# Optimization experiments

Hardware: AMD Instinct MI355X
Metric: run time of the kernel (lower is better)

## Reference

```python
import jax, jax.numpy as jnp
import numpy as np

N_NODES = 100000
N_EDGES = 600000
D_IN = 128
D_OUT = 512  # hidden_size * gates_num = 128 * 4


def setup_inputs() -> dict:
    key = jax.random.key(0)
    k1, k2, k3, k4 = jax.random.split(key, 4)
    x = jax.random.normal(k1, (N_NODES, D_IN), dtype=jnp.float32)
    edge_index = jax.random.randint(k2, (2, N_EDGES), 0, N_NODES, dtype=jnp.int64)
    W = jax.random.normal(k3, (D_OUT, D_IN), dtype=jnp.float32) * (1.0 / np.sqrt(D_IN))
    b = jax.random.normal(k4, (D_OUT,), dtype=jnp.float32) * 0.01
    return {"x": x, "edge_index": edge_index, "W": W, "b": b}


def reference(x, edge_index, W, b):
    row, col = edge_index[0], edge_index[1]
    # gather neighbor features and scatter-add into destination nodes
    agg = jax.ops.segment_sum(x[col], row, num_segments=x.shape[0])  # [N, D_IN]
    out = x + agg  # residual
    return out @ W.T + b  # [N, D_OUT]
```

## Files before the change

kernel.cpp:

```cpp
#include <hip/hip_runtime.h>
#include <hip/hip_bf16.h>

#define N_NODES 100000
#define N_EDGES 600000
#define D_IN 128
#define D_OUT 512
#define CAP 40
#define OVF_CAP 1024

typedef __bf16 bf16x8 __attribute__((ext_vector_type(8)));
typedef __bf16 bf16x2 __attribute__((ext_vector_type(2)));
typedef float f32x4 __attribute__((ext_vector_type(4)));

#define OFF_CNT   25600000
#define OFF_OVFC  26000000
#define OFF_OVF   26000016
#define OFF_BUCK  26008208

__global__ void k_bucket(const int* __restrict__ ei, int* __restrict__ cnt,
                         int* __restrict__ bucket, int* __restrict__ ovf_cnt,
                         int2* __restrict__ ovf) {
    int e = blockIdx.x * blockDim.x + threadIdx.x;
    if (e >= N_EDGES) return;
    int r = ei[e];
    int c = ei[N_EDGES + e];
    int slot = atomicAdd(&cnt[r], 1);
    if (slot < CAP) {
        bucket[(size_t)r * CAP + slot] = c;
    } else {
        int oi = atomicAdd(ovf_cnt, 1);
        if (oi < OVF_CAP) ovf[oi] = make_int2(r, c);
    }
}

__global__ void k_agg(const float* __restrict__ x, const int* __restrict__ cnt,
                      const int* __restrict__ bucket, const int* __restrict__ ovf_cnt,
                      const int2* __restrict__ ovf, __bf16* __restrict__ h) {
    int gw = (blockIdx.x * blockDim.x + threadIdx.x) >> 6;
    if (gw >= N_NODES) return;
    int lane = threadIdx.x & 63;
    const float2* xr = (const float2*)x;

    float2 a0 = xr[(size_t)gw * 64 + lane];
    float ax1 = 0.f, ay1 = 0.f, ax2 = 0.f, ay2 = 0.f, ax3 = 0.f, ay3 = 0.f;

    int deg = __builtin_amdgcn_readfirstlane(cnt[gw]);
    int dmin = deg < CAP ? deg : CAP;
    const int* bk = bucket + (size_t)gw * CAP;

    int myc = (lane < dmin) ? bk[lane] : 0;

    int d = 0;
    for (; d + 3 < dmin; d += 4) {
        int c0 = __builtin_amdgcn_readlane(myc, d);
        int c1 = __builtin_amdgcn_readlane(myc, d + 1);
        int c2 = __builtin_amdgcn_readlane(myc, d + 2);
        int c3 = __builtin_amdgcn_readlane(myc, d + 3);
        float2 v0 = xr[(size_t)c0 * 64 + lane];
        float2 v1 = xr[(size_t)c1 * 64 + lane];
        float2 v2 = xr[(size_t)c2 * 64 + lane];
        float2 v3 = xr[(size_t)c3 * 64 + lane];
        a0.x += v0.x; a0.y += v0.y;
        ax1 += v1.x;  ay1 += v1.y;
        ax2 += v2.x;  ay2 += v2.y;
        ax3 += v3.x;  ay3 += v3.y;
    }
    for (; d < dmin; ++d) {
        int c0 = __builtin_amdgcn_readlane(myc, d);
        float2 v0 = xr[(size_t)c0 * 64 + lane];
        a0.x += v0.x; a0.y += v0.y;
    }
    a0.x += ax1 + ax2 + ax3;
    a0.y += ay1 + ay2 + ay3;

    if (deg > CAP) {
        int n = *ovf_cnt;
        if (n > OVF_CAP) n = OVF_CAP;
        for (int i = 0; i < n; ++i) {
            int2 e = ovf[i];
            if (e.x == gw) {
                float2 v = xr[(size_t)e.y * 64 + lane];
                a0.x += v.x; a0.y += v.y;
            }
        }
    }

    bf16x2 o = { (__bf16)a0.x, (__bf16)a0.y };
    ((bf16x2*)h)[(size_t)gw * 64 + lane] = o;
}

#define BM 128
#define BN 128
#define LDA 136
#define LDB 136
#define NWG 3128

__device__ inline bf16x8 cvt8(float4 v0, float4 v1) {
    bf16x8 u = { (__bf16)v0.x, (__bf16)v0.y, (__bf16)v0.z, (__bf16)v0.w,
                 (__bf16)v1.x, (__bf16)v1.y, (__bf16)v1.z, (__bf16)v1.w };
    return u;
}

__launch_bounds__(512, 4)
__global__ void k_gemm(const __bf16* __restrict__ h, const float* __restrict__ W,
                       const float* __restrict__ bias, float* __restrict__ out) {
    __shared__ __bf16 As[BM * LDA];
    __shared__ __bf16 Bs[BN * LDB];

    int tid = threadIdx.x;

    int bid = blockIdx.x;
    int wg = (bid & 7) * (NWG / 8) + (bid >> 3);
    int m0 = (wg >> 2) * BM;
    int n0 = (wg & 3) * BN;

    #pragma unroll
    for (int it = 0; it < 4; ++it) {
        int i = tid + it * 512;
        int r = i >> 4;
        int c = (i & 15) << 3;
        int gr = m0 + r;
        if (gr > N_NODES - 1) gr = N_NODES - 1;
        *(bf16x8*)&As[r * LDA + c] = *(const bf16x8*)(h + (size_t)gr * D_IN + c);
    }
    #pragma unroll
    for (int it = 0; it < 4; ++it) {
        int i = tid + it * 512;
        int r = i >> 4;
        int c = (i & 15) << 3;
        const float* src = W + (size_t)(n0 + r) * D_IN + c;
        float4 v0 = *(const float4*)(src);
        float4 v1 = *(const float4*)(src + 4);
        *(bf16x8*)&Bs[r * LDB + c] = cvt8(v0, v1);
    }
    __syncthreads();

    int lane = tid & 63;
    int wave = tid >> 6;
    int wm = wave & 1;
    int wn = wave >> 1;
    int quad = lane >> 4;
    int l16 = lane & 15;

    f32x4 acc[4][2] = {};

    const __bf16* Abase = &As[(wm * 64 + l16) * LDA + quad * 8];
    const __bf16* Bbase = &Bs[(wn * 32 + l16) * LDB + quad * 8];

    #pragma unroll
    for (int ks = 0; ks < 4; ++ks) {
        bf16x8 a0 = *(const bf16x8*)(Abase + ks * 32);
        bf16x8 a1 = *(const bf16x8*)(Abase + 16 * LDA + ks * 32);
        bf16x8 a2 = *(const bf16x8*)(Abase + 32 * LDA + ks * 32);
        bf16x8 a3 = *(const bf16x8*)(Abase + 48 * LDA + ks * 32);
        bf16x8 b0 = *(const bf16x8*)(Bbase + ks * 32);
        bf16x8 b1 = *(const bf16x8*)(Bbase + 16 * LDB + ks * 32);
        acc[0][0] = __builtin_amdgcn_mfma_f32_16x16x32_bf16(a0, b0, acc[0][0], 0, 0, 0);
        acc[0][1] = __builtin_amdgcn_mfma_f32_16x16x32_bf16(a0, b1, acc[0][1], 0, 0, 0);
        acc[1][0] = __builtin_amdgcn_mfma_f32_16x16x32_bf16(a1, b0, acc[1][0], 0, 0, 0);
        acc[1][1] = __builtin_amdgcn_mfma_f32_16x16x32_bf16(a1, b1, acc[1][1], 0, 0, 0);
        acc[2][0] = __builtin_amdgcn_mfma_f32_16x16x32_bf16(a2, b0, acc[2][0], 0, 0, 0);
        acc[2][1] = __builtin_amdgcn_mfma_f32_16x16x32_bf16(a2, b1, acc[2][1], 0, 0, 0);
        acc[3][0] = __builtin_amdgcn_mfma_f32_16x16x32_bf16(a3, b0, acc[3][0], 0, 0, 0);
        acc[3][1] = __builtin_amdgcn_mfma_f32_16x16x32_bf16(a3, b1, acc[3][1], 0, 0, 0);
    }

    float bias0 = bias[n0 + wn * 32 + l16];
    float bias1 = bias[n0 + wn * 32 + 16 + l16];
    #pragma unroll
    for (int mt = 0; mt < 4; ++mt) {
        int mrow = m0 + wm * 64 + mt * 16 + quad * 4;
        #pragma unroll
        for (int nt = 0; nt < 2; ++nt) {
            int ncol = n0 + wn * 32 + nt * 16 + l16;
            float bv = nt ? bias1 : bias0;
            #pragma unroll
            for (int rg = 0; rg < 4; ++rg) {
                int m = mrow + rg;
                if (m < N_NODES)
                    out[(size_t)m * D_OUT + ncol] = acc[mt][nt][rg] + bv;
            }
        }
    }
}

extern "C" void kernel_launch(void* const* d_in, const int* in_sizes, int n_in,
                              void* d_out, int out_size, void* d_ws, size_t ws_size,
                              hipStream_t stream) {
    const float* x  = (const float*)d_in[0];
    const int*   ei = (const int*)d_in[1];
    const float* W  = (const float*)d_in[2];
    const float* b  = (const float*)d_in[3];
    float* out = (float*)d_out;

    char* ws = (char*)d_ws;
    __bf16* h    = (__bf16*)ws;
    int* cnt     = (int*)(ws + OFF_CNT);
    int* ovf_cnt = (int*)(ws + OFF_OVFC);
    int2* ovf    = (int2*)(ws + OFF_OVF);
    int* bucket  = (int*)(ws + OFF_BUCK);

    hipMemsetAsync(cnt, 0, (OFF_OVFC - OFF_CNT) + 16, stream);

    k_bucket<<<(N_EDGES + 255) / 256, 256, 0, stream>>>(ei, cnt, bucket, ovf_cnt, ovf);
    k_agg<<<(N_NODES * 64 + 255) / 256, 256, 0, stream>>>(x, cnt, bucket, ovf_cnt, ovf, h);
    k_gemm<<<NWG, 512, 0, stream>>>(h, W, b, out);
}
```

Measured before the change: 372.6 us.

## Pre-convert x and W to bf16 so neighbor gathers read half the bytes

The bucketing kernel gains extra blocks that convert x and W to bf16 copies in workspace. The aggregation then gathers neighbor rows as bf16, halving the bytes per random gather, and the GEMM loads pre-converted W. The cost is an extra streaming pass over x (read fp32, write bf16) and a small loss of precision in neighbor features before accumulation.

```diff
diff --git a/kernel.cpp b/kernel.cpp
--- a/kernel.cpp
+++ b/kernel.cpp
@@ -16,30 +16,58 @@
 #define OFF_OVFC  26000000
 #define OFF_OVF   26000016
 #define OFF_BUCK  26008208
-
-__global__ void k_bucket(const int* __restrict__ ei, int* __restrict__ cnt,
-                         int* __restrict__ bucket, int* __restrict__ ovf_cnt,
-                         int2* __restrict__ ovf) {
-    int e = blockIdx.x * blockDim.x + threadIdx.x;
-    if (e >= N_EDGES) return;
-    int r = ei[e];
-    int c = ei[N_EDGES + e];
-    int slot = atomicAdd(&cnt[r], 1);
-    if (slot < CAP) {
-        bucket[(size_t)r * CAP + slot] = c;
+#define OFF_XB    42008208
+#define OFF_WB    67608208
+
+__device__ inline bf16x8 cvt8(float4 v0, float4 v1) {
+    bf16x8 u = { (__bf16)v0.x, (__bf16)v0.y, (__bf16)v0.z, (__bf16)v0.w,
+                 (__bf16)v1.x, (__bf16)v1.y, (__bf16)v1.z, (__bf16)v1.w };
+    return u;
+}
+
+#define EB  2344
+#define XB  6250
+#define WBK 32
+__global__ void k_bucket_cvt(const int* __restrict__ ei, const float* __restrict__ x,
+                             const float* __restrict__ W, int* __restrict__ cnt,
+                             int* __restrict__ bucket, int* __restrict__ ovf_cnt,
+                             int2* __restrict__ ovf, __bf16* __restrict__ xb,
+                             __bf16* __restrict__ wb) {
+    int b = blockIdx.x;
+    if (b < EB) {
+        int e = b * 256 + threadIdx.x;
+        if (e >= N_EDGES) return;
+        int r = ei[e];
+        int c = ei[N_EDGES + e];
+        int slot = atomicAdd(&cnt[r], 1);
+        if (slot < CAP) {
+            bucket[(size_t)r * CAP + slot] = c;
+        } else {
+            int oi = atomicAdd(ovf_cnt, 1);
+            if (oi < OVF_CAP) ovf[oi] = make_int2(r, c);
+        }
+    } else if (b < EB + XB) {
+        size_t i = (size_t)(b - EB) * 2048 + threadIdx.x * 8;
+        float4 v0 = *(const float4*)(x + i);
+        float4 v1 = *(const float4*)(x + i + 4);
+        *(bf16x8*)(xb + i) = cvt8(v0, v1);
     } else {
-        int oi = atomicAdd(ovf_cnt, 1);
-        if (oi < OVF_CAP) ovf[oi] = make_int2(r, c);
-    }
-}
-
-__global__ void k_agg(const float* __restrict__ x, const int* __restrict__ cnt,
-                      const int* __restrict__ bucket, const int* __restrict__ ovf_cnt,
-                      const int2* __restrict__ ovf, __bf16* __restrict__ h) {
+        size_t i = (size_t)(b - EB - XB) * 2048 + threadIdx.x * 8;
+        float4 v0 = *(const float4*)(W + i);
+        float4 v1 = *(const float4*)(W + i + 4);
+        *(bf16x8*)(wb + i) = cvt8(v0, v1);
+    }
+}
+
+__global__ void k_agg(const float* __restrict__ x, const __bf16* __restrict__ xb,
+                      const int* __restrict__ cnt, const int* __restrict__ bucket,
+                      const int* __restrict__ ovf_cnt, const int2* __restrict__ ovf,
+                      __bf16* __restrict__ h) {
     int gw = (blockIdx.x * blockDim.x + threadIdx.x) >> 6;
     if (gw >= N_NODES) return;
     int lane = threadIdx.x & 63;
     const float2* xr = (const float2*)x;
+    const unsigned int* xbu = (const unsigned int*)xb;
 
     float2 a0 = xr[(size_t)gw * 64 + lane];
     float ax1 = 0.f, ay1 = 0.f, ax2 = 0.f, ay2 = 0.f, ax3 = 0.f, ay3 = 0.f;
@@ -56,19 +84,24 @@
         int c1 = __builtin_amdgcn_readlane(myc, d + 1);
         int c2 = __builtin_amdgcn_readlane(myc, d + 2);
         int c3 = __builtin_amdgcn_readlane(myc, d + 3);
-        float2 v0 = xr[(size_t)c0 * 64 + lane];
-        float2 v1 = xr[(size_t)c1 * 64 + lane];
-        float2 v2 = xr[(size_t)c2 * 64 + lane];
-        float2 v3 = xr[(size_t)c3 * 64 + lane];
-        a0.x += v0.x; a0.y += v0.y;
-        ax1 += v1.x;  ay1 += v1.y;
-        ax2 += v2.x;  ay2 += v2.y;
-        ax3 += v3.x;  ay3 += v3.y;
+        unsigned int u0 = xbu[(size_t)c0 * 64 + lane];
+        unsigned int u1 = xbu[(size_t)c1 * 64 + lane];
+        unsigned int u2 = xbu[(size_t)c2 * 64 + lane];
+        unsigned int u3 = xbu[(size_t)c3 * 64 + lane];
+        a0.x += __uint_as_float(u0 << 16);
+        a0.y += __uint_as_float(u0 & 0xffff0000u);
+        ax1  += __uint_as_float(u1 << 16);
+        ay1  += __uint_as_float(u1 & 0xffff0000u);
+        ax2  += __uint_as_float(u2 << 16);
+        ay2  += __uint_as_float(u2 & 0xffff0000u);
+        ax3  += __uint_as_float(u3 << 16);
+        ay3  += __uint_as_float(u3 & 0xffff0000u);
     }
     for (; d < dmin; ++d) {
         int c0 = __builtin_amdgcn_readlane(myc, d);
-        float2 v0 = xr[(size_t)c0 * 64 + lane];
-        a0.x += v0.x; a0.y += v0.y;
+        unsigned int u0 = xbu[(size_t)c0 * 64 + lane];
+        a0.x += __uint_as_float(u0 << 16);
+        a0.y += __uint_as_float(u0 & 0xffff0000u);
     }
     a0.x += ax1 + ax2 + ax3;
     a0.y += ay1 + ay2 + ay3;
@@ -95,14 +128,8 @@
 #define LDB 136
 #define NWG 3128
 
-__device__ inline bf16x8 cvt8(float4 v0, float4 v1) {
-    bf16x8 u = { (__bf16)v0.x, (__bf16)v0.y, (__bf16)v0.z, (__bf16)v0.w,
-                 (__bf16)v1.x, (__bf16)v1.y, (__bf16)v1.z, (__bf16)v1.w };
-    return u;
-}
-
 __launch_bounds__(512, 4)
-__global__ void k_gemm(const __bf16* __restrict__ h, const float* __restrict__ W,
+__global__ void k_gemm(const __bf16* __restrict__ h, const __bf16* __restrict__ wb,
                        const float* __restrict__ bias, float* __restrict__ out) {
     __shared__ __bf16 As[BM * LDA];
     __shared__ __bf16 Bs[BN * LDB];
@@ -128,10 +155,7 @@
         int i = tid + it * 512;
         int r = i >> 4;
         int c = (i & 15) << 3;
-        const float* src = W + (size_t)(n0 + r) * D_IN + c;
-        float4 v0 = *(const float4*)(src);
-        float4 v1 = *(const float4*)(src + 4);
-        *(bf16x8*)&Bs[r * LDB + c] = cvt8(v0, v1);
+        *(bf16x8*)&Bs[r * LDB + c] = *(const bf16x8*)(wb + (size_t)(n0 + r) * D_IN + c);
     }
     __syncthreads();
 
@@ -199,10 +223,14 @@
     int* ovf_cnt = (int*)(ws + OFF_OVFC);
     int2* ovf    = (int2*)(ws + OFF_OVF);
     int* bucket  = (int*)(ws + OFF_BUCK);
+    __bf16* xb   = (__bf16*)(ws + OFF_XB);
+    __bf16* wb   = (__bf16*)(ws + OFF_WB);
 
     hipMemsetAsync(cnt, 0, (OFF_OVFC - OFF_CNT) + 16, stream);
 
-    k_bucket<<<(N_EDGES + 255) / 256, 256, 0, stream>>>(ei, cnt, bucket, ovf_cnt, ovf);
-    k_agg<<<(N_NODES * 64 + 255) / 256, 256, 0, stream>>>(x, cnt, bucket, ovf_cnt, ovf, h);
-    k_gemm<<<NWG, 512, 0, stream>>>(h, W, b, out);
-}
+    k_bucket_cvt<<<EB + XB + WBK, 256, 0, stream>>>(ei, x, W, cnt, bucket,
+                                                    ovf_cnt, ovf, xb, wb);
+    k_agg<<<(N_NODES * 64 + 255) / 256, 256, 0, stream>>>(x, xb, cnt, bucket,
+                                                          ovf_cnt, ovf, h);
+    k_gemm<<<NWG, 512, 0, stream>>>(h, wb, b, out);
+}
```

Measured after the change: 373.7 us. No clear change (+0.3%).
